# Kernel optimization log

Measured on AMD Instinct MI355X. Metric: run time of the kernel, lower is better.

The kernel has to match this reference:

```python
import jax, jax.numpy as jnp
import numpy as np
from jax import lax


def _kaiming_uniform(key, shape):
    fan_in = shape[1]
    bound = np.sqrt(6.0 / fan_in)
    return jax.random.uniform(key, shape, jnp.float32, -bound, bound)


def rbf_conv(x, w, k, pad):
    # x: [B,C,H,W]; w: [O, C*k*k]. Equivalent to F.unfold + torch.cdist (p=2).
    patches = lax.conv_general_dilated_patches(
        x, (k, k), (1, 1), [(pad, pad), (pad, pad)])  # [B, C*k*k, Ho, Wo]
    B, D, Ho, Wo = patches.shape
    p = patches.reshape(B, D, Ho * Wo)                 # [B, D, L]
    pn = jnp.sum(p * p, axis=1)                        # [B, L]
    wn = jnp.sum(w * w, axis=1)                        # [O]
    cross = jnp.einsum('bdl,od->bol', p, w)            # [B, O, L]
    d2 = pn[:, None, :] + wn[None, :, None] - 2.0 * cross
    d = jnp.sqrt(jnp.maximum(d2, 0.0))
    return d.reshape(B, w.shape[0], Ho, Wo)


def sfm(x, alpha):
    # non-overlapping (fh,fw) blocks, elementwise alpha weight, mean-pool
    B, C, H, W = x.shape
    fh, fw = alpha.shape
    xb = x.reshape(B, C, H // fh, fh, W // fw, fw).transpose(0, 1, 2, 4, 3, 5)
    return jnp.mean(xb * alpha, axis=(-2, -1))         # [B,C,H//fh,W//fw]


def gauss_act(d, std):
    return jnp.exp(d * d / (-2.0 * std * std))


def crelu(x, bias):
    return x * (x >= bias).astype(x.dtype)


def basic_block(x, w, std, bias, alpha, k, pad):
    d = rbf_conv(x, w, k, pad)
    return sfm(crelu(gauss_act(d, std), bias), alpha)


def setup_inputs() -> dict:
    key = jax.random.key(0)
    ks = jax.random.split(key, 8)
    x = jax.random.normal(ks[0], (16, 3, 128, 128), jnp.float32)
    w1 = _kaiming_uniform(ks[1], (96, 3 * 5 * 5))
    w2 = _kaiming_uniform(ks[2], (192, 96 * 5 * 5))
    w3 = _kaiming_uniform(ks[3], (384, 192 * 3 * 3))
    alpha = jnp.linspace(0.9, 0.99, 4, dtype=jnp.float32).reshape(2, 2)
    fc_w = jax.random.normal(ks[4], (100, 384 * 32 * 32), jnp.float32) * 0.01
    fc_b = jnp.zeros((100,), jnp.float32)
    return {
        'x': x,
        'w1': w1, 'std1': jnp.array([2.0], jnp.float32), 'bias1': jnp.array([0.3], jnp.float32), 'alpha1': alpha,
        'w2': w2, 'std2': jnp.array([2.0], jnp.float32), 'bias2': jnp.array([0.3], jnp.float32), 'alpha2': alpha,
        'w3': w3, 'std3': jnp.array([2.0], jnp.float32), 'bias3': jnp.array([0.3], jnp.float32),
        'fc_w': fc_w, 'fc_b': fc_b,
    }


def reference(x, w1, std1, bias1, alpha1, w2, std2, bias2, alpha2,
              w3, std3, bias3, fc_w, fc_b):
    h = basic_block(x, w1, std1, bias1, alpha1, 5, 2)      # [16,96,64,64]
    h = basic_block(h, w2, std2, bias2, alpha2, 5, 2)      # [16,192,32,32]
    d = rbf_conv(h, w3, 3, 1)                              # [16,384,32,32]
    h = crelu(gauss_act(d, std3), bias3)
    out = h.reshape(x.shape[0], -1) @ fc_w.T + fc_b        # [16,100]
    return out
```

## Files before the change

### kernel.cpp

```cpp
#include <hip/hip_runtime.h>

#define TPB 256

typedef short bf16x8 __attribute__((ext_vector_type(8)));
typedef float f32x4 __attribute__((ext_vector_type(4)));

__device__ inline unsigned short f2bf(float f) {
    unsigned int u = __float_as_uint(f);
    unsigned int r = (u + 0x7fffu + ((u >> 16) & 1u)) >> 16;
    return (unsigned short)r;
}
__device__ inline float bf2f(unsigned short h) {
    return __uint_as_float(((unsigned int)h) << 16);
}

__device__ __forceinline__ void gl16(void* lds, const void* g) {
    __builtin_amdgcn_global_load_lds(
        (const __attribute__((address_space(1))) unsigned int*)g,
        (__attribute__((address_space(3))) unsigned int*)lds, 16, 0, 0);
}

__global__ void prep_all(const float* __restrict__ x,
                         const float* __restrict__ w1, const float* __restrict__ w2,
                         const float* __restrict__ w3,
                         unsigned short* __restrict__ xbf,
                         unsigned short* __restrict__ w1r, unsigned short* __restrict__ w2r,
                         unsigned short* __restrict__ w3r, unsigned short* __restrict__ zerob,
                         float* __restrict__ wn1, float* __restrict__ wn2,
                         float* __restrict__ wn3) {
    int bid = blockIdx.x;
    int tid = threadIdx.x;
    if (bid < 1024) {
        int idx = bid * TPB + tid;
        int b = idx >> 14, px = idx & 16383;
        const float* xb = x + (size_t)b * 3 * 16384 + px;
        float v0 = xb[0], v1 = xb[16384], v2 = xb[32768];
        ushort4 v;
        v.x = f2bf(v0); v.y = f2bf(v1); v.z = f2bf(v2);
        v.w = f2bf(v0 * v0 + v1 * v1 + v2 * v2);
        *(ushort4*)&xbf[(size_t)idx * 4] = v;
    } else if (bid < 4388) {
        int idx = (bid - 1024) * TPB + tid;
        if (idx < 13056) {
            int o = idx / 136, d = idx - o * 136;
            int tp = d >> 2, c = d & 3;
            float v = 0.f;
            if (tp < 30) {
                int ki = tp / 6, kj = tp - 6 * ki;
                if (kj < 5) v = (c < 3) ? w1[o * 75 + c * 25 + ki * 5 + kj] : -0.5f;
            }
            w1r[idx] = f2bf(v);
        } else if (idx < 492288) {
            int i = idx - 13056;
            int c = i & 31; int r = i >> 5;
            int o = r % 192; r /= 192;
            int tap = r % 26; int cg = r / 26;
            float v = 0.f;
            if (tap < 25) v = w2[((size_t)o * 96 + cg * 32 + c) * 25 + tap];
            w2r[i] = f2bf(v);
        } else if (idx < 860928) {
            int i = idx - 492288;
            int c = i & 31; int r = i >> 5;
            int o = r % 192; r /= 192;
            int tap = r % 10; int cg = r / 10;
            float v = 0.f;
            if (tap < 9) v = w3[((size_t)o * 192 + cg * 32 + c) * 9 + tap];
            w3r[i] = f2bf(v);
        } else if (idx < 860992) {
            zerob[idx - 860928] = 0;
        }
    } else {
        int o = (bid - 4388) * 4 + (tid >> 6);
        int lane = tid & 63;
        const float* row; float* dst; int D;
        if (o < 96)       { row = w1 + (size_t)o * 75;           D = 75;   dst = wn1 + o; }
        else if (o < 288) { int r = o - 96;  row = w2 + (size_t)r * 2400; D = 2400; dst = wn2 + r; }
        else              { int r = o - 288; row = w3 + (size_t)r * 1728; D = 1728; dst = wn3 + r; }
        float acc = 0.f;
        for (int i = lane; i < D; i += 64) { float v = row[i]; acc += v * v; }
        #pragma unroll
        for (int off = 32; off >= 1; off >>= 1) acc += __shfl_down(acc, off);
        if (lane == 0) *dst = acc;
    }
}

__launch_bounds__(256, 2)
__global__ void conv1_mfma(const unsigned short* __restrict__ xbf,
                           const unsigned short* __restrict__ w1r,
                           const float* __restrict__ wn,
                           const float* __restrict__ stdp, const float* __restrict__ biasp,
                           const float* __restrict__ alphap,
                           unsigned short* __restrict__ out,
                           float* __restrict__ sqout)
{
    __shared__ unsigned short in_s[22 * 20 * 4];
    __shared__ unsigned short w_s[96 * 136];

    int bid = blockIdx.x;
    int tx = bid & 7; bid >>= 3;
    int ty = bid & 7; bid >>= 3;
    int b = bid;
    int x0 = tx * 16, y0 = ty * 16;
    int tid = threadIdx.x;
    int lane = tid & 63, wv = tid >> 6;
    int col = lane & 15, kg = lane >> 4;

    for (int idx = tid; idx < 21 * 20; idx += 256) {
        int py = idx / 20, px = idx - py * 20;
        int gy = y0 - 2 + py, gx = x0 - 2 + px;
        ushort4 v = make_ushort4(0, 0, 0, 0);
        if (gy >= 0 && gy < 128 && gx >= 0 && gx < 128)
            v = *(const ushort4*)&xbf[(((size_t)b * 128 + gy) * 128 + gx) * 4];
        *(ushort4*)&in_s[idx * 4] = v;
    }
    for (int idx = tid; idx < 1632; idx += 256)
        *(bf16x8*)&w_s[idx * 8] = *(const bf16x8*)&w1r[idx * 8];
    __syncthreads();

    f32x4 acc[6][4];
    #pragma unroll
    for (int mt = 0; mt < 6; ++mt)
        #pragma unroll
        for (int n = 0; n < 4; ++n) acc[mt][n] = (f32x4){0.f, 0.f, 0.f, 0.f};

    #pragma unroll
    for (int ks = 0; ks < 4; ++ks) {
        int tap0 = ks * 8 + kg * 2;
        int ki = tap0 / 6, kj = tap0 - 6 * ki;
        bf16x8 bfrag[4];
        #pragma unroll
        for (int n = 0; n < 4; ++n) {
            int row = wv * 4 + n + ki;
            int ix = col + kj;
            const unsigned short* p = &in_s[(row * 20 + ix) * 4];
            union { bf16x8 v; uint2 u[2]; } tmp;
            tmp.u[0] = *(const uint2*)p;
            tmp.u[1] = *(const uint2*)(p + 4);
            bfrag[n] = tmp.v;
        }
        bf16x8 afrag[6];
        #pragma unroll
        for (int mt = 0; mt < 6; ++mt)
            afrag[mt] = *(const bf16x8*)&w_s[(mt * 16 + col) * 136 + ks * 32 + kg * 8];
        #pragma unroll
        for (int mt = 0; mt < 6; ++mt)
            #pragma unroll
            for (int n = 0; n < 4; ++n)
                acc[mt][n] = __builtin_amdgcn_mfma_f32_16x16x32_bf16(
                    afrag[mt], bfrag[n], acc[mt][n], 0, 0, 0);
    }

    float stdv = stdp[0], biasv = biasp[0];
    float inv2s2 = 1.f / (2.f * stdv * stdv);
    float a00 = alphap[0], a01 = alphap[1], a10 = alphap[2], a11 = alphap[3];
    int dx = col & 1;
    float ax0 = dx ? a01 : a00;
    float ax1 = dx ? a11 : a10;

    float sqa[2] = {0.f, 0.f};
    #pragma unroll
    for (int mt = 0; mt < 6; ++mt) {
        #pragma unroll
        for (int p2 = 0; p2 < 2; ++p2) {
            unsigned short res[4];
            #pragma unroll
            for (int r = 0; r < 4; ++r) {
                int o = mt * 16 + kg * 4 + r;
                float wno = wn[o];
                float d20 = fmaxf(wno - 2.f * acc[mt][2 * p2][r], 0.f);
                float d21 = fmaxf(wno - 2.f * acc[mt][2 * p2 + 1][r], 0.f);
                float g0 = __expf(-d20 * inv2s2);
                float g1 = __expf(-d21 * inv2s2);
                g0 = (g0 >= biasv) ? g0 : 0.f;
                g1 = (g1 >= biasv) ? g1 : 0.f;
                float s = ax0 * g0 + ax1 * g1;
                s += __shfl_xor(s, 1);
                res[r] = f2bf(0.25f * s);
                float vv = bf2f(res[r]);
                sqa[p2] += vv * vv;
            }
            if (dx == 0) {
                int yo = ty * 8 + wv * 2 + p2, xo = tx * 8 + (col >> 1);
                *(ushort4*)&out[(((size_t)b * 64 + yo) * 64 + xo) * 96 + mt * 16 + kg * 4] =
                    make_ushort4(res[0], res[1], res[2], res[3]);
            }
        }
    }
    #pragma unroll
    for (int p2 = 0; p2 < 2; ++p2) {
        float s = sqa[p2];
        s += __shfl_xor(s, 16);
        s += __shfl_xor(s, 32);
        if (dx == 0 && kg == 0) {
            int yo = ty * 8 + wv * 2 + p2, xo = tx * 8 + (col >> 1);
            sqout[((size_t)b * 64 + yo) * 64 + xo] = s;
        }
    }
}

__launch_bounds__(256, 2)
__global__ void conv2_mfma(const unsigned short* __restrict__ hin,
                           const unsigned short* __restrict__ wt2,
                           const float* __restrict__ sq1,
                           const float* __restrict__ wn,
                           const float* __restrict__ stdp, const float* __restrict__ biasp,
                           const float* __restrict__ alphap,
                           const unsigned short* __restrict__ zerob,
                           unsigned short* __restrict__ hout)
{
    __shared__ unsigned short in_s[240 * 32];
    __shared__ unsigned short w_s[2][2 * 192 * 32];
    __shared__ float sq_s[240];
    __shared__ int s_nz[4];

    int bid = blockIdx.x;
    int xt = bid & 3; bid >>= 2;
    int yt = bid & 7; bid >>= 3;
    int b = bid;
    int x0 = xt * 16, y0 = yt * 8;
    int tid = threadIdx.x;
    int lane = tid & 63, wid = tid >> 6;
    int wave_m = wid >> 1, wave_n = wid & 1;
    int col = lane & 15, kg = lane >> 4;
    int coly = col >> 3, colx = col & 7;

    if (tid < 240) {
        int r = tid / 20, c = tid - r * 20;
        int gy = y0 - 2 + r, gx = x0 - 2 + c;
        float v = 0.f;
        if (gy >= 0 && gy < 64 && gx >= 0 && gx < 64)
            v = sq1[((size_t)b * 64 + gy) * 64 + gx];
        sq_s[tid] = v;
    }

    f32x4 acc[6][4];
    #pragma unroll
    for (int mt = 0; mt < 6; ++mt)
        #pragma unroll
        for (int nt = 0; nt < 4; ++nt) acc[mt][nt] = (f32x4){0.f, 0.f, 0.f, 0.f};

    for (int cg = 0; cg < 3; ++cg) {
        #pragma unroll
        for (int i = 0; i < 4; ++i) {
            int chunk = tid + i * 256;
            if (chunk < 960) {
                int px = chunk >> 2, c16 = chunk & 3;
                int iy = px / 20, ix = px - iy * 20;
                int gy = y0 - 2 + iy, gx = x0 - 2 + ix;
                const void* src = (gy >= 0 && gy < 64 && gx >= 0 && gx < 64)
                    ? (const void*)&hin[(((size_t)b * 64 + gy) * 64 + gx) * 96 + cg * 32 + c16 * 8]
                    : (const void*)zerob;
                gl16(&in_s[chunk * 8], src);
            }
        }
        __syncthreads();

        unsigned int nzb = 0;
        #pragma unroll
        for (int i = 0; i < 4; ++i) {
            int chunk = tid + i * 256;
            if (chunk < 960) {
                uint4 v = *(const uint4*)&in_s[chunk * 8];
                nzb |= v.x | v.y | v.z | v.w;
            }
        }
        bool any = __any(nzb != 0);
        if (lane == 0) s_nz[wid] = any ? 1 : 0;
        __syncthreads();
        if (s_nz[0] | s_nz[1] | s_nz[2] | s_nz[3]) {
            #pragma unroll
            for (int i = 0; i < 6; ++i) {
                int chunk = tid + i * 256;
                int tp = chunk / 768, rem = chunk - tp * 768;
                gl16(&w_s[0][tp * 6144 + rem * 8],
                     &wt2[(((size_t)cg * 26 + tp) * 192) * 32 + rem * 8]);
            }
            __syncthreads();
            for (int pr = 0; pr < 13; ++pr) {
                int cur = pr & 1;
                if (pr < 12) {
                    #pragma unroll
                    for (int i = 0; i < 6; ++i) {
                        int chunk = tid + i * 256;
                        int tp = chunk / 768, rem = chunk - tp * 768;
                        gl16(&w_s[cur ^ 1][tp * 6144 + rem * 8],
                             &wt2[(((size_t)cg * 26 + (pr + 1) * 2 + tp) * 192) * 32 + rem * 8]);
                    }
                }
                #pragma unroll
                for (int t2 = 0; t2 < 2; ++t2) {
                    int tap = pr * 2 + t2;
                    int ki = tap / 5, kj = tap - 5 * ki;
                    if (tap >= 25) { ki = 0; kj = 0; }
                    bf16x8 bfrag[4], afrag[6];
                    #pragma unroll
                    for (int nt = 0; nt < 4; ++nt) {
                        int yy = 2 * nt + coly + ki;
                        int xx = wave_n * 8 + colx + kj;
                        bfrag[nt] = *(const bf16x8*)&in_s[(yy * 20 + xx) * 32 + kg * 8];
                    }
                    #pragma unroll
                    for (int mt = 0; mt < 6; ++mt)
                        afrag[mt] = *(const bf16x8*)
                            &w_s[cur][t2 * 6144 + (wave_m * 96 + mt * 16 + col) * 32 + kg * 8];
                    #pragma unroll
                    for (int mt = 0; mt < 6; ++mt)
                        #pragma unroll
                        for (int nt = 0; nt < 4; ++nt)
                            acc[mt][nt] = __builtin_amdgcn_mfma_f32_16x16x32_bf16(
                                afrag[mt], bfrag[nt], acc[mt][nt], 0, 0, 0);
                }
                __syncthreads();
            }
        }
    }

    float stdv = stdp[0], biasv = biasp[0];
    float inv2s2 = 1.f / (2.f * stdv * stdv);
    float a_own = alphap[coly * 2 + (col & 1)];
    #pragma unroll
    for (int nt = 0; nt < 4; ++nt) {
        int ly = 2 * nt + coly + 2;
        int lx = wave_n * 8 + colx + 2;
        float pnv = 0.f;
        #pragma unroll
        for (int dy = -2; dy <= 2; ++dy)
            #pragma unroll
            for (int dx2 = -2; dx2 <= 2; ++dx2)
                pnv += sq_s[(ly + dy) * 20 + (lx + dx2)];
        int x = x0 + wave_n * 8 + colx;
        int yo = (y0 >> 1) + nt;
        int xo = x >> 1;
        #pragma unroll
        for (int mt = 0; mt < 6; ++mt) {
            int ob = wave_m * 96 + mt * 16 + (kg << 2);
            unsigned short res[4];
            #pragma unroll
            for (int r = 0; r < 4; ++r) {
                float d2 = fmaxf(pnv + wn[ob + r] - 2.f * acc[mt][nt][r], 0.f);
                float g = __expf(-d2 * inv2s2);
                g = (g >= biasv) ? g : 0.f;
                g *= a_own;
                g += __shfl_xor(g, 1);
                g += __shfl_xor(g, 8);
                res[r] = f2bf(0.25f * g);
            }
            if (((col & 1) == 0) && ((col & 8) == 0)) {
                *(ushort4*)&hout[(((size_t)b * 32 + yo) * 32 + xo) * 192 + ob] =
                    make_ushort4(res[0], res[1], res[2], res[3]);
            }
        }
    }
}

__launch_bounds__(256, 2)
__global__ void conv3_mfma(const unsigned short* __restrict__ hin,
                           const unsigned short* __restrict__ wt3,
                           const float* __restrict__ wn,
                           const float* __restrict__ stdp, const float* __restrict__ biasp,
                           const unsigned short* __restrict__ zerob,
                           unsigned short* __restrict__ hout)
{
    __shared__ unsigned short in_s[180 * 32];
    __shared__ unsigned short w_s[2][2 * 96 * 32];
    __shared__ float pnacc[180];

    int bid = blockIdx.x;
    int sp = bid & 7; bid >>= 3;
    int ot = bid & 3; int b = bid >> 2;
    int x0 = (sp & 1) * 16, y0 = (sp >> 1) * 8, o0 = ot * 96;
    int tid = threadIdx.x;
    int lane = tid & 63, wid = tid >> 6;
    int om = wid >> 1, wn2 = wid & 1;
    int col = lane & 15, kg = lane >> 4;
    int coly = col >> 3, colx = col & 7;

    if (tid < 180) pnacc[tid] = 0.f;

    f32x4 acc[3][4];
    #pragma unroll
    for (int mt = 0; mt < 3; ++mt)
        #pragma unroll
        for (int nt = 0; nt < 4; ++nt) acc[mt][nt] = (f32x4){0.f, 0.f, 0.f, 0.f};

    for (int cg = 0; cg < 6; ++cg) {
        #pragma unroll
        for (int i = 0; i < 3; ++i) {
            int chunk = tid + i * 256;
            if (chunk < 720) {
                int px = chunk >> 2, c16 = chunk & 3;
                int iy = px / 18, ix = px - iy * 18;
                int gy = y0 - 1 + iy, gx = x0 - 1 + ix;
                const void* src = (gy >= 0 && gy < 32 && gx >= 0 && gx < 32)
                    ? (const void*)&hin[(((size_t)b * 32 + gy) * 32 + gx) * 192 + cg * 32 + c16 * 8]
                    : (const void*)zerob;
                gl16(&in_s[chunk * 8], src);
            }
        }
        #pragma unroll
        for (int i = 0; i < 3; ++i) {
            int chunk = tid + i * 256;
            int tp = chunk / 384, rem = chunk - tp * 384;
            gl16(&w_s[0][tp * 3072 + rem * 8],
                 &wt3[(((size_t)cg * 10 + tp) * 192 + o0) * 32 + rem * 8]);
        }
        __syncthreads();

        if (tid < 180) {
            const unsigned short* p = &in_s[tid * 32];
            float a = 0.f;
            #pragma unroll
            for (int c = 0; c < 32; c += 8) {
                bf16x8 v = *(const bf16x8*)&p[c];
                #pragma unroll
                for (int j = 0; j < 8; ++j) { float f = bf2f((unsigned short)v[j]); a += f * f; }
            }
            pnacc[tid] += a;
        }

        for (int pr = 0; pr < 5; ++pr) {
            int cur = pr & 1;
            if (pr < 4) {
                #pragma unroll
                for (int i = 0; i < 3; ++i) {
                    int chunk = tid + i * 256;
                    int tp = chunk / 384, rem = chunk - tp * 384;
                    gl16(&w_s[cur ^ 1][tp * 3072 + rem * 8],
                         &wt3[(((size_t)cg * 10 + (pr + 1) * 2 + tp) * 192 + o0) * 32 + rem * 8]);
                }
            }
            #pragma unroll
            for (int t2 = 0; t2 < 2; ++t2) {
                int tap = pr * 2 + t2;
                int ki = tap / 3, kj = tap - 3 * ki;
                if (tap >= 9) { ki = 0; kj = 0; }
                bf16x8 bfrag[4], afrag[3];
                #pragma unroll
                for (int nt = 0; nt < 4; ++nt) {
                    int yy = 2 * nt + coly + ki;
                    int xx = wn2 * 8 + colx + kj;
                    bfrag[nt] = *(const bf16x8*)&in_s[(yy * 18 + xx) * 32 + kg * 8];
                }
                #pragma unroll
                for (int mt = 0; mt < 3; ++mt)
                    afrag[mt] = *(const bf16x8*)
                        &w_s[cur][(t2 * 96 + om * 48 + mt * 16 + col) * 32 + kg * 8];
                #pragma unroll
                for (int mt = 0; mt < 3; ++mt)
                    #pragma unroll
                    for (int nt = 0; nt < 4; ++nt)
                        acc[mt][nt] = __builtin_amdgcn_mfma_f32_16x16x32_bf16(
                            afrag[mt], bfrag[nt], acc[mt][nt], 0, 0, 0);
            }
            __syncthreads();
        }
    }

    float stdv = stdp[0], biasv = biasp[0];
    float inv2s2 = 1.f / (2.f * stdv * stdv);
    #pragma unroll
    for (int nt = 0; nt < 4; ++nt) {
        int y = y0 + 2 * nt + coly;
        int x = x0 + wn2 * 8 + colx;
        int ly = 2 * nt + coly + 1, lx = wn2 * 8 + colx + 1;
        float pnv = 0.f;
        #pragma unroll
        for (int dy = -1; dy <= 1; ++dy)
            #pragma unroll
            for (int dx = -1; dx <= 1; ++dx)
                pnv += pnacc[(ly + dy) * 18 + (lx + dx)];
        #pragma unroll
        for (int mt = 0; mt < 3; ++mt) {
            int ob = o0 + om * 48 + mt * 16 + (kg << 2);
            #pragma unroll
            for (int r = 0; r < 4; ++r) {
                float d2 = fmaxf(pnv + wn[ob + r] - 2.f * acc[mt][nt][r], 0.f);
                float g = __expf(-d2 * inv2s2);
                g = (g >= biasv) ? g : 0.f;
                hout[((size_t)b * 384 + ob + r) * 1024 + y * 32 + x] = f2bf(g);
            }
        }
    }
}

__launch_bounds__(256, 4)
__global__ void fc_mfma(const unsigned short* __restrict__ h3bf,
                        const float* __restrict__ fw,
                        float* __restrict__ fcp,
                        int* __restrict__ flags)
{
    __shared__ unsigned short h3s[16 * 520];
    __shared__ unsigned short fws[16 * 520];
    __shared__ float red[4][16][16];
    __shared__ int s_nz[4];
    const size_t KI = 393216;
    int ch = blockIdx.x;
    int i0 = ch * 512;
    int tid = threadIdx.x;
    int lane = tid & 63, wv = tid >> 6;
    int col = lane & 15, kg = lane >> 4;

    unsigned int nzbits = 0;
    #pragma unroll
    for (int it = 0; it < 4; ++it) {
        int c = tid + it * 256;
        int b = c >> 6, off = (c & 63) * 8;
        bf16x8 v = *(const bf16x8*)&h3bf[(size_t)b * KI + i0 + off];
        union { bf16x8 s; unsigned int u[4]; } cv; cv.s = v;
        nzbits |= cv.u[0] | cv.u[1] | cv.u[2] | cv.u[3];
        *(bf16x8*)&h3s[b * 520 + off] = v;
    }
    bool any = __any(nzbits != 0);
    if (lane == 0) s_nz[wv] = any ? 1 : 0;
    __syncthreads();
    int anyall = s_nz[0] | s_nz[1] | s_nz[2] | s_nz[3];
    if (!anyall) {
        if (tid == 0) flags[ch] = 0;
        return;
    }
    if (tid == 0) flags[ch] = 1;

    float4 pre[8];
    #pragma unroll
    for (int it = 0; it < 8; ++it) {
        int c = tid + it * 256;
        int row = c >> 7, off4 = (c & 127) * 4;
        pre[it] = (row < 100) ? *(const float4*)&fw[(size_t)row * KI + i0 + off4]
                              : make_float4(0.f, 0.f, 0.f, 0.f);
    }

    for (int jt = 0; jt < 7; ++jt) {
        int j0 = jt * 16;
        #pragma unroll
        for (int it = 0; it < 8; ++it) {
            int c = tid + it * 256;
            int row = c >> 7, off4 = (c & 127) * 4;
            *(ushort4*)&fws[row * 520 + off4] =
                make_ushort4(f2bf(pre[it].x), f2bf(pre[it].y), f2bf(pre[it].z), f2bf(pre[it].w));
        }
        if (jt < 6) {
            #pragma unroll
            for (int it = 0; it < 8; ++it) {
                int c = tid + it * 256;
                int row = c >> 7, off4 = (c & 127) * 4;
                int j = j0 + 16 + row;
                pre[it] = (j < 100) ? *(const float4*)&fw[(size_t)j * KI + i0 + off4]
                                    : make_float4(0.f, 0.f, 0.f, 0.f);
            }
        }
        __syncthreads();
        f32x4 acc = (f32x4){0.f, 0.f, 0.f, 0.f};
        #pragma unroll
        for (int s = 0; s < 4; ++s) {
            int k = wv * 128 + s * 32 + kg * 8;
            bf16x8 af = *(const bf16x8*)&fws[col * 520 + k];
            bf16x8 bg = *(const bf16x8*)&h3s[col * 520 + k];
            acc = __builtin_amdgcn_mfma_f32_16x16x32_bf16(af, bg, acc, 0, 0, 0);
        }
        #pragma unroll
        for (int r = 0; r < 4; ++r) red[wv][kg * 4 + r][col] = acc[r];
        __syncthreads();
        int j = tid >> 4, bb = tid & 15;
        float s = red[0][j][bb] + red[1][j][bb] + red[2][j][bb] + red[3][j][bb];
        fcp[((size_t)ch * 112 + j0 + j) * 16 + bb] = s;
    }
}

__global__ void fc_final(const float* __restrict__ fcp, const int* __restrict__ flags,
                         const float* __restrict__ fb, float* __restrict__ outp) {
    int j = blockIdx.x;
    int lane = threadIdx.x;
    float acc[16];
    #pragma unroll
    for (int b = 0; b < 16; ++b) acc[b] = 0.f;
    for (int ch = lane; ch < 768; ch += 64) {
        if (flags[ch]) {
            const float* p = &fcp[((size_t)ch * 112 + j) * 16];
            #pragma unroll
            for (int b = 0; b < 16; ++b) acc[b] += p[b];
        }
    }
    #pragma unroll
    for (int off = 32; off >= 1; off >>= 1)
        #pragma unroll
        for (int b = 0; b < 16; ++b) acc[b] += __shfl_down(acc[b], off);
    if (lane == 0) {
        float bj = fb[j];
        #pragma unroll
        for (int b = 0; b < 16; ++b) outp[b * 100 + j] = bj + acc[b];
    }
}

extern "C" void kernel_launch(void* const* d_in, const int* in_sizes, int n_in,
                              void* d_out, int out_size, void* d_ws, size_t ws_size,
                              hipStream_t stream) {
    const float* x      = (const float*)d_in[0];
    const float* w1     = (const float*)d_in[1];
    const float* std1   = (const float*)d_in[2];
    const float* bias1  = (const float*)d_in[3];
    const float* alpha1 = (const float*)d_in[4];
    const float* w2     = (const float*)d_in[5];
    const float* std2   = (const float*)d_in[6];
    const float* bias2  = (const float*)d_in[7];
    const float* alpha2 = (const float*)d_in[8];
    const float* w3     = (const float*)d_in[9];
    const float* std3   = (const float*)d_in[10];
    const float* bias3  = (const float*)d_in[11];
    const float* fc_w   = (const float*)d_in[12];
    const float* fc_b   = (const float*)d_in[13];
    float* out = (float*)d_out;
    float* ws  = (float*)d_ws;

    float* sbuf  = ws;
    float* fcp   = sbuf + 65536;
    float* wn1   = fcp + 1376256;
    float* wn2   = wn1 + 96;
    float* wn3   = wn2 + 192;
    int*   flags = (int*)(wn3 + 384);
    float* rest  = wn3 + 384 + 768 + 32;
    unsigned short* h1bf = (unsigned short*)rest;
    unsigned short* h2bf = h1bf + 6291456;
    unsigned short* h3bf = h2bf + 3145728;
    unsigned short* xbf  = h3bf + 6291456;
    unsigned short* w1r  = xbf + 1048576;
    unsigned short* w2r  = w1r + 13056;
    unsigned short* w3r  = w2r + 479232;
    unsigned short* zerob = w3r + 368640;

    dim3 B(TPB);

    prep_all<<<dim3(4556), B, 0, stream>>>(x, w1, w2, w3, xbf, w1r, w2r, w3r, zerob,
                                           wn1, wn2, wn3);

    conv1_mfma<<<dim3(1024), B, 0, stream>>>(xbf, w1r, wn1, std1, bias1, alpha1,
                                             h1bf, sbuf);

    conv2_mfma<<<dim3(512), B, 0, stream>>>(
        h1bf, w2r, sbuf, wn2, std2, bias2, alpha2, zerob, h2bf);

    conv3_mfma<<<dim3(512), B, 0, stream>>>(
        h2bf, w3r, wn3, std3, bias3, zerob, h3bf);

    fc_mfma<<<dim3(768), B, 0, stream>>>(h3bf, fc_w, fcp, flags);
    fc_final<<<dim3(100), dim3(64), 0, stream>>>(fcp, flags, fc_b, out);
}
```

Before: 100.9 us.

## Fuse all stages into one cooperative persistent kernel with grid syncs

Replaces the six separate kernel launches with a single cooperative megakernel of 512 blocks that runs prep, conv1, conv2, conv3, fc and the final reduction, using grid.sync between stages. Shared memory becomes one byte buffer carved per stage. The goal is to remove launch gaps and tail effects between kernels. In exchange, every stage runs with a fixed grid and occupancy, and the per-stage LDS is sized to the largest stage. If the cooperative launch fails, it falls back to separate kernels.

```diff
diff --git a/kernel.cpp b/kernel.cpp
--- a/kernel.cpp
+++ b/kernel.cpp
@@ -1,4 +1,7 @@
 #include <hip/hip_runtime.h>
+#include <hip/hip_cooperative_groups.h>
+
+namespace cg = cooperative_groups;
 
 #define TPB 256
 
@@ -20,28 +23,26 @@
         (__attribute__((address_space(3))) unsigned int*)lds, 16, 0, 0);
 }
 
-__global__ void prep_all(const float* __restrict__ x,
-                         const float* __restrict__ w1, const float* __restrict__ w2,
-                         const float* __restrict__ w3,
-                         unsigned short* __restrict__ xbf,
-                         unsigned short* __restrict__ w1r, unsigned short* __restrict__ w2r,
-                         unsigned short* __restrict__ w3r, unsigned short* __restrict__ zerob,
-                         float* __restrict__ wn1, float* __restrict__ wn2,
-                         float* __restrict__ wn3) {
-    int bid = blockIdx.x;
-    int tid = threadIdx.x;
-    if (bid < 1024) {
-        int idx = bid * TPB + tid;
-        int b = idx >> 14, px = idx & 16383;
-        const float* xb = x + (size_t)b * 3 * 16384 + px;
-        float v0 = xb[0], v1 = xb[16384], v2 = xb[32768];
-        ushort4 v;
-        v.x = f2bf(v0); v.y = f2bf(v1); v.z = f2bf(v2);
-        v.w = f2bf(v0 * v0 + v1 * v1 + v2 * v2);
-        *(ushort4*)&xbf[(size_t)idx * 4] = v;
-    } else if (bid < 4388) {
-        int idx = (bid - 1024) * TPB + tid;
-        if (idx < 13056) {
+
+__device__ __forceinline__ void dev_prep(int gi, int stride,
+    const float* __restrict__ x, const float* __restrict__ w1,
+    const float* __restrict__ w2, const float* __restrict__ w3,
+    unsigned short* __restrict__ xbf, unsigned short* __restrict__ w1r,
+    unsigned short* __restrict__ w2r, unsigned short* __restrict__ w3r,
+    unsigned short* __restrict__ zerob)
+{
+    const int NX = 262144, E1 = NX + 13056, E2 = E1 + 479232, E3 = E2 + 368640, TOT = E3 + 64;
+    for (int i = gi; i < TOT; i += stride) {
+        if (i < NX) {
+            int b = i >> 14, px = i & 16383;
+            const float* xb = x + (size_t)b * 49152 + px;
+            float v0 = xb[0], v1 = xb[16384], v2 = xb[32768];
+            ushort4 v;
+            v.x = f2bf(v0); v.y = f2bf(v1); v.z = f2bf(v2);
+            v.w = f2bf(v0 * v0 + v1 * v1 + v2 * v2);
+            *(ushort4*)&xbf[(size_t)i * 4] = v;
+        } else if (i < E1) {
+            int idx = i - NX;
             int o = idx / 136, d = idx - o * 136;
             int tp = d >> 2, c = d & 3;
             float v = 0.f;
@@ -50,58 +51,59 @@
                 if (kj < 5) v = (c < 3) ? w1[o * 75 + c * 25 + ki * 5 + kj] : -0.5f;
             }
             w1r[idx] = f2bf(v);
-        } else if (idx < 492288) {
-            int i = idx - 13056;
-            int c = i & 31; int r = i >> 5;
+        } else if (i < E2) {
+            int idx = i - E1;
+            int c = idx & 31; int r = idx >> 5;
             int o = r % 192; r /= 192;
-            int tap = r % 26; int cg = r / 26;
+            int tap = r % 26; int cgx = r / 26;
             float v = 0.f;
-            if (tap < 25) v = w2[((size_t)o * 96 + cg * 32 + c) * 25 + tap];
-            w2r[i] = f2bf(v);
-        } else if (idx < 860928) {
-            int i = idx - 492288;
-            int c = i & 31; int r = i >> 5;
+            if (tap < 25) v = w2[((size_t)o * 96 + cgx * 32 + c) * 25 + tap];
+            w2r[idx] = f2bf(v);
+        } else if (i < E3) {
+            int idx = i - E2;
+            int c = idx & 31; int r = idx >> 5;
             int o = r % 192; r /= 192;
-            int tap = r % 10; int cg = r / 10;
+            int tap = r % 10; int cgx = r / 10;
             float v = 0.f;
-            if (tap < 9) v = w3[((size_t)o * 192 + cg * 32 + c) * 9 + tap];
-            w3r[i] = f2bf(v);
-        } else if (idx < 860992) {
-            zerob[idx - 860928] = 0;
-        }
-    } else {
-        int o = (bid - 4388) * 4 + (tid >> 6);
-        int lane = tid & 63;
-        const float* row; float* dst; int D;
-        if (o < 96)       { row = w1 + (size_t)o * 75;           D = 75;   dst = wn1 + o; }
-        else if (o < 288) { int r = o - 96;  row = w2 + (size_t)r * 2400; D = 2400; dst = wn2 + r; }
-        else              { int r = o - 288; row = w3 + (size_t)r * 1728; D = 1728; dst = wn3 + r; }
-        float acc = 0.f;
-        for (int i = lane; i < D; i += 64) { float v = row[i]; acc += v * v; }
-        #pragma unroll
-        for (int off = 32; off >= 1; off >>= 1) acc += __shfl_down(acc, off);
-        if (lane == 0) *dst = acc;
-    }
-}
-
-__launch_bounds__(256, 2)
-__global__ void conv1_mfma(const unsigned short* __restrict__ xbf,
-                           const unsigned short* __restrict__ w1r,
-                           const float* __restrict__ wn,
-                           const float* __restrict__ stdp, const float* __restrict__ biasp,
-                           const float* __restrict__ alphap,
-                           unsigned short* __restrict__ out,
-                           float* __restrict__ sqout)
+            if (tap < 9) v = w3[((size_t)o * 192 + cgx * 32 + c) * 9 + tap];
+            w3r[idx] = f2bf(v);
+        } else {
+            zerob[i - E3] = 0;
+        }
+    }
+}
+
+__device__ __forceinline__ void dev_wn(int o, int lane,
+    const float* __restrict__ w1, const float* __restrict__ w2,
+    const float* __restrict__ w3,
+    float* __restrict__ wn1, float* __restrict__ wn2, float* __restrict__ wn3)
 {
-    __shared__ unsigned short in_s[22 * 20 * 4];
-    __shared__ unsigned short w_s[96 * 136];
-
-    int bid = blockIdx.x;
-    int tx = bid & 7; bid >>= 3;
-    int ty = bid & 7; bid >>= 3;
-    int b = bid;
+    const float* row; float* dst; int D;
+    if (o < 96)       { row = w1 + (size_t)o * 75;           D = 75;   dst = wn1 + o; }
+    else if (o < 288) { int r = o - 96;  row = w2 + (size_t)r * 2400; D = 2400; dst = wn2 + r; }
+    else              { int r = o - 288; row = w3 + (size_t)r * 1728; D = 1728; dst = wn3 + r; }
+    float acc = 0.f;
+    for (int i = lane; i < D; i += 64) { float v = row[i]; acc += v * v; }
+    #pragma unroll
+    for (int off = 32; off >= 1; off >>= 1) acc += __shfl_down(acc, off);
+    if (lane == 0) *dst = acc;
+}
+
+__device__ __forceinline__ void dev_conv1(int t, int tid, unsigned char* smem,
+    const unsigned short* __restrict__ xbf, const unsigned short* __restrict__ w1r,
+    const float* __restrict__ wn,
+    const float* __restrict__ stdp, const float* __restrict__ biasp,
+    const float* __restrict__ alphap,
+    unsigned short* __restrict__ out, float* __restrict__ sqout)
+{
+    unsigned short* in_s = (unsigned short*)smem;
+    unsigned short* w_s  = (unsigned short*)(smem + 3520);
+    __syncthreads();
+
+    int tx = t & 7; t >>= 3;
+    int ty = t & 7; t >>= 3;
+    int b = t;
     int x0 = tx * 16, y0 = ty * 16;
-    int tid = threadIdx.x;
     int lane = tid & 63, wv = tid >> 6;
     int col = lane & 15, kg = lane >> 4;
 
@@ -198,27 +200,22 @@
     }
 }
 
-__launch_bounds__(256, 2)
-__global__ void conv2_mfma(const unsigned short* __restrict__ hin,
-                           const unsigned short* __restrict__ wt2,
-                           const float* __restrict__ sq1,
-                           const float* __restrict__ wn,
-                           const float* __restrict__ stdp, const float* __restrict__ biasp,
-                           const float* __restrict__ alphap,
-                           const unsigned short* __restrict__ zerob,
-                           unsigned short* __restrict__ hout)
+__device__ __forceinline__ void dev_conv2(int t, int tid, unsigned char* smem,
+    const unsigned short* __restrict__ hin, const unsigned short* __restrict__ wt2,
+    const float* __restrict__ sq1, const float* __restrict__ wn,
+    const float* __restrict__ stdp, const float* __restrict__ biasp,
+    const float* __restrict__ alphap, const unsigned short* __restrict__ zerob,
+    unsigned short* __restrict__ hout)
 {
-    __shared__ unsigned short in_s[240 * 32];
-    __shared__ unsigned short w_s[2][2 * 192 * 32];
-    __shared__ float sq_s[240];
-    __shared__ int s_nz[4];
-
-    int bid = blockIdx.x;
-    int xt = bid & 3; bid >>= 2;
-    int yt = bid & 7; bid >>= 3;
-    int b = bid;
+    unsigned short* in_s = (unsigned short*)smem;
+    unsigned short* w_s  = (unsigned short*)(smem + 15360);
+    float* sq_s          = (float*)(smem + 64512);
+    int* s_nz            = (int*)(smem + 65472);
+
+    int xt = t & 3; t >>= 2;
+    int yt = t & 7; t >>= 3;
+    int b = t;
     int x0 = xt * 16, y0 = yt * 8;
-    int tid = threadIdx.x;
     int lane = tid & 63, wid = tid >> 6;
     int wave_m = wid >> 1, wave_n = wid & 1;
     int col = lane & 15, kg = lane >> 4;
@@ -239,7 +236,7 @@
         #pragma unroll
         for (int nt = 0; nt < 4; ++nt) acc[mt][nt] = (f32x4){0.f, 0.f, 0.f, 0.f};
 
-    for (int cg = 0; cg < 3; ++cg) {
+    for (int cgx = 0; cgx < 3; ++cgx) {
         #pragma unroll
         for (int i = 0; i < 4; ++i) {
             int chunk = tid + i * 256;
@@ -248,7 +245,7 @@
                 int iy = px / 20, ix = px - iy * 20;
                 int gy = y0 - 2 + iy, gx = x0 - 2 + ix;
                 const void* src = (gy >= 0 && gy < 64 && gx >= 0 && gx < 64)
-                    ? (const void*)&hin[(((size_t)b * 64 + gy) * 64 + gx) * 96 + cg * 32 + c16 * 8]
+                    ? (const void*)&hin[(((size_t)b * 64 + gy) * 64 + gx) * 96 + cgx * 32 + c16 * 8]
                     : (const void*)zerob;
                 gl16(&in_s[chunk * 8], src);
             }
@@ -272,8 +269,8 @@
             for (int i = 0; i < 6; ++i) {
                 int chunk = tid + i * 256;
                 int tp = chunk / 768, rem = chunk - tp * 768;
-                gl16(&w_s[0][tp * 6144 + rem * 8],
-                     &wt2[(((size_t)cg * 26 + tp) * 192) * 32 + rem * 8]);
+                gl16(&w_s[tp * 6144 + rem * 8],
+                     &wt2[(((size_t)cgx * 26 + tp) * 192) * 32 + rem * 8]);
             }
             __syncthreads();
             for (int pr = 0; pr < 13; ++pr) {
@@ -283,8 +280,8 @@
                     for (int i = 0; i < 6; ++i) {
                         int chunk = tid + i * 256;
                         int tp = chunk / 768, rem = chunk - tp * 768;
-                        gl16(&w_s[cur ^ 1][tp * 6144 + rem * 8],
-                             &wt2[(((size_t)cg * 26 + (pr + 1) * 2 + tp) * 192) * 32 + rem * 8]);
+                        gl16(&w_s[(cur ^ 1) * 12288 + tp * 6144 + rem * 8],
+                             &wt2[(((size_t)cgx * 26 + (pr + 1) * 2 + tp) * 192) * 32 + rem * 8]);
                     }
                 }
                 #pragma unroll
@@ -302,7 +299,7 @@
                     #pragma unroll
                     for (int mt = 0; mt < 6; ++mt)
                         afrag[mt] = *(const bf16x8*)
-                            &w_s[cur][t2 * 6144 + (wave_m * 96 + mt * 16 + col) * 32 + kg * 8];
+                            &w_s[cur * 12288 + t2 * 6144 + (wave_m * 96 + mt * 16 + col) * 32 + kg * 8];
                     #pragma unroll
                     for (int mt = 0; mt < 6; ++mt)
                         #pragma unroll
@@ -353,23 +350,19 @@
     }
 }
 
-__launch_bounds__(256, 2)
-__global__ void conv3_mfma(const unsigned short* __restrict__ hin,
-                           const unsigned short* __restrict__ wt3,
-                           const float* __restrict__ wn,
-                           const float* __restrict__ stdp, const float* __restrict__ biasp,
-                           const unsigned short* __restrict__ zerob,
-                           unsigned short* __restrict__ hout)
+__device__ __forceinline__ void dev_conv3(int t, int tid, unsigned char* smem,
+    const unsigned short* __restrict__ hin, const unsigned short* __restrict__ wt3,
+    const float* __restrict__ wn,
+    const float* __restrict__ stdp, const float* __restrict__ biasp,
+    const unsigned short* __restrict__ zerob, unsigned short* __restrict__ hout)
 {
-    __shared__ unsigned short in_s[180 * 32];
-    __shared__ unsigned short w_s[2][2 * 96 * 32];
-    __shared__ float pnacc[180];
-
-    int bid = blockIdx.x;
-    int sp = bid & 7; bid >>= 3;
-    int ot = bid & 3; int b = bid >> 2;
+    unsigned short* in_s = (unsigned short*)smem;
+    unsigned short* w_s  = (unsigned short*)(smem + 11520);
+    float* pnacc         = (float*)(smem + 36096);
+
+    int sp = t & 7; t >>= 3;
+    int ot = t & 3; int b = t >> 2;
     int x0 = (sp & 1) * 16, y0 = (sp >> 1) * 8, o0 = ot * 96;
-    int tid = threadIdx.x;
     int lane = tid & 63, wid = tid >> 6;
     int om = wid >> 1, wn2 = wid & 1;
     int col = lane & 15, kg = lane >> 4;
@@ -383,7 +376,7 @@
         #pragma unroll
         for (int nt = 0; nt < 4; ++nt) acc[mt][nt] = (f32x4){0.f, 0.f, 0.f, 0.f};
 
-    for (int cg = 0; cg < 6; ++cg) {
+    for (int cgx = 0; cgx < 6; ++cgx) {
         #pragma unroll
         for (int i = 0; i < 3; ++i) {
             int chunk = tid + i * 256;
@@ -392,7 +385,7 @@
                 int iy = px / 18, ix = px - iy * 18;
                 int gy = y0 - 1 + iy, gx = x0 - 1 + ix;
                 const void* src = (gy >= 0 && gy < 32 && gx >= 0 && gx < 32)
-                    ? (const void*)&hin[(((size_t)b * 32 + gy) * 32 + gx) * 192 + cg * 32 + c16 * 8]
+                    ? (const void*)&hin[(((size_t)b * 32 + gy) * 32 + gx) * 192 + cgx * 32 + c16 * 8]
                     : (const void*)zerob;
                 gl16(&in_s[chunk * 8], src);
             }
@@ -401,8 +394,8 @@
         for (int i = 0; i < 3; ++i) {
             int chunk = tid + i * 256;
             int tp = chunk / 384, rem = chunk - tp * 384;
-            gl16(&w_s[0][tp * 3072 + rem * 8],
-                 &wt3[(((size_t)cg * 10 + tp) * 192 + o0) * 32 + rem * 8]);
+            gl16(&w_s[tp * 3072 + rem * 8],
+                 &wt3[(((size_t)cgx * 10 + tp) * 192 + o0) * 32 + rem * 8]);
         }
         __syncthreads();
 
@@ -425,8 +418,8 @@
                 for (int i = 0; i < 3; ++i) {
                     int chunk = tid + i * 256;
                     int tp = chunk / 384, rem = chunk - tp * 384;
-                    gl16(&w_s[cur ^ 1][tp * 3072 + rem * 8],
-                         &wt3[(((size_t)cg * 10 + (pr + 1) * 2 + tp) * 192 + o0) * 32 + rem * 8]);
+                    gl16(&w_s[(cur ^ 1) * 6144 + tp * 3072 + rem * 8],
+                         &wt3[(((size_t)cgx * 10 + (pr + 1) * 2 + tp) * 192 + o0) * 32 + rem * 8]);
                 }
             }
             #pragma unroll
@@ -444,7 +437,7 @@
                 #pragma unroll
                 for (int mt = 0; mt < 3; ++mt)
                     afrag[mt] = *(const bf16x8*)
-                        &w_s[cur][(t2 * 96 + om * 48 + mt * 16 + col) * 32 + kg * 8];
+                        &w_s[cur * 6144 + t2 * 3072 + (om * 48 + mt * 16 + col) * 32 + kg * 8];
                 #pragma unroll
                 for (int mt = 0; mt < 3; ++mt)
                     #pragma unroll
@@ -483,20 +476,18 @@
     }
 }
 
-__launch_bounds__(256, 4)
-__global__ void fc_mfma(const unsigned short* __restrict__ h3bf,
-                        const float* __restrict__ fw,
-                        float* __restrict__ fcp,
-                        int* __restrict__ flags)
+__device__ __forceinline__ void dev_fc(int ch, int tid, unsigned char* smem,
+    const unsigned short* __restrict__ h3bf, const float* __restrict__ fw,
+    float* __restrict__ fcp, int* __restrict__ flags)
 {
-    __shared__ unsigned short h3s[16 * 520];
-    __shared__ unsigned short fws[16 * 520];
-    __shared__ float red[4][16][16];
-    __shared__ int s_nz[4];
+    unsigned short* h3s = (unsigned short*)smem;
+    unsigned short* fws = (unsigned short*)(smem + 16640);
+    float* red          = (float*)(smem + 33280);
+    int* s_nz           = (int*)(smem + 37376);
+    __syncthreads();
+
     const size_t KI = 393216;
-    int ch = blockIdx.x;
     int i0 = ch * 512;
-    int tid = threadIdx.x;
     int lane = tid & 63, wv = tid >> 6;
     int col = lane & 15, kg = lane >> 4;
 
@@ -558,18 +549,19 @@
             acc = __builtin_amdgcn_mfma_f32_16x16x32_bf16(af, bg, acc, 0, 0, 0);
         }
         #pragma unroll
-        for (int r = 0; r < 4; ++r) red[wv][kg * 4 + r][col] = acc[r];
+        for (int r = 0; r < 4; ++r) red[wv * 256 + (kg * 4 + r) * 16 + col] = acc[r];
         __syncthreads();
         int j = tid >> 4, bb = tid & 15;
-        float s = red[0][j][bb] + red[1][j][bb] + red[2][j][bb] + red[3][j][bb];
+        float s = red[0 * 256 + j * 16 + bb] + red[1 * 256 + j * 16 + bb] +
+                  red[2 * 256 + j * 16 + bb] + red[3 * 256 + j * 16 + bb];
         fcp[((size_t)ch * 112 + j0 + j) * 16 + bb] = s;
     }
 }
 
-__global__ void fc_final(const float* __restrict__ fcp, const int* __restrict__ flags,
-                         const float* __restrict__ fb, float* __restrict__ outp) {
-    int j = blockIdx.x;
-    int lane = threadIdx.x;
+__device__ __forceinline__ void dev_final(int j, int lane,
+    const float* __restrict__ fcp, const int* __restrict__ flags,
+    const float* __restrict__ fb, float* __restrict__ outp)
+{
     float acc[16];
     #pragma unroll
     for (int b = 0; b < 16; ++b) acc[b] = 0.f;
@@ -589,6 +581,93 @@
         #pragma unroll
         for (int b = 0; b < 16; ++b) outp[b * 100 + j] = bj + acc[b];
     }
+}
+
+__launch_bounds__(256, 2)
+__global__ void mega(const float* x, const float* w1, const float* w2, const float* w3,
+                     const float* std1, const float* bias1, const float* alpha1,
+                     const float* std2, const float* bias2, const float* alpha2,
+                     const float* std3, const float* bias3,
+                     const float* fc_w, const float* fc_b, float* out,
+                     float* sbuf, float* fcp, float* wn1, float* wn2, float* wn3,
+                     int* flags,
+                     unsigned short* h1bf, unsigned short* h2bf, unsigned short* h3bf,
+                     unsigned short* xbf, unsigned short* w1r, unsigned short* w2r,
+                     unsigned short* w3r, unsigned short* zerob)
+{
+    __shared__ __align__(16) unsigned char smem[65488];
+    cg::grid_group grid = cg::this_grid();
+    int bid = blockIdx.x;
+    int tid = threadIdx.x;
+
+    dev_prep(bid * 256 + tid, 512 * 256, x, w1, w2, w3, xbf, w1r, w2r, w3r, zerob);
+    if (bid < 168) dev_wn(bid * 4 + (tid >> 6), tid & 63, w1, w2, w3, wn1, wn2, wn3);
+    grid.sync();
+
+    for (int t = bid; t < 1024; t += 512)
+        dev_conv1(t, tid, smem, xbf, w1r, wn1, std1, bias1, alpha1, h1bf, sbuf);
+    grid.sync();
+
+    dev_conv2(bid, tid, smem, h1bf, w2r, sbuf, wn2, std2, bias2, alpha2, zerob, h2bf);
+    grid.sync();
+
+    dev_conv3(bid, tid, smem, h2bf, w3r, wn3, std3, bias3, zerob, h3bf);
+    grid.sync();
+
+    for (int ch = bid; ch < 768; ch += 512)
+        dev_fc(ch, tid, smem, h3bf, fc_w, fcp, flags);
+    grid.sync();
+
+    if (bid < 100 && tid < 64)
+        dev_final(bid, tid, fcp, flags, fc_b, out);
+}
+
+__launch_bounds__(256)
+__global__ void k_prep(const float* x, const float* w1, const float* w2, const float* w3,
+                       unsigned short* xbf, unsigned short* w1r, unsigned short* w2r,
+                       unsigned short* w3r, unsigned short* zerob,
+                       float* wn1, float* wn2, float* wn3) {
+    dev_prep(blockIdx.x * 256 + threadIdx.x, 2048 * 256, x, w1, w2, w3,
+             xbf, w1r, w2r, w3r, zerob);
+    if (blockIdx.x < 168)
+        dev_wn(blockIdx.x * 4 + (threadIdx.x >> 6), threadIdx.x & 63,
+               w1, w2, w3, wn1, wn2, wn3);
+}
+
+__launch_bounds__(256, 2)
+__global__ void k_conv1(const unsigned short* xbf, const unsigned short* w1r,
+                        const float* wn, const float* stdp, const float* biasp,
+                        const float* alphap, unsigned short* out, float* sqout) {
+    __shared__ __align__(16) unsigned char smem[29696];
+    dev_conv1(blockIdx.x, threadIdx.x, smem, xbf, w1r, wn, stdp, biasp, alphap, out, sqout);
+}
+
+__launch_bounds__(256, 2)
+__global__ void k_conv2(const unsigned short* hin, const unsigned short* wt2,
+                        const float* sq1, const float* wn, const float* stdp,
+                        const float* biasp, const float* alphap,
+                        const unsigned short* zerob, unsigned short* hout) {
+    __shared__ __align__(16) unsigned char smem[65488];
+    dev_conv2(blockIdx.x, threadIdx.x, smem, hin, wt2, sq1, wn, stdp, biasp, alphap,
+              zerob, hout);
+}
+
+__launch_bounds__(256, 2)
+__global__ void k_conv3(const unsigned short* hin, const unsigned short* wt3,
+                        const float* wn, const float* stdp, const float* biasp,
+                        const unsigned short* zerob, unsigned short* hout) {
+    __shared__ __align__(16) unsigned char smem[36864];
+    dev_conv3(blockIdx.x, threadIdx.x, smem, hin, wt3, wn, stdp, biasp, zerob, hout);
+}
+
+__launch_bounds__(256, 2)
+__global__ void k_fc(const unsigned short* h3bf, const float* fw, float* fcp, int* flags) {
+    __shared__ __align__(16) unsigned char smem[37392];
+    dev_fc(blockIdx.x, threadIdx.x, smem, h3bf, fw, fcp, flags);
+}
+
+__global__ void k_final(const float* fcp, const int* flags, const float* fb, float* outp) {
+    dev_final(blockIdx.x, threadIdx.x, fcp, flags, fb, outp);
 }
 
 extern "C" void kernel_launch(void* const* d_in, const int* in_sizes, int n_in,
@@ -627,20 +706,29 @@
     unsigned short* w3r  = w2r + 479232;
     unsigned short* zerob = w3r + 368640;
 
-    dim3 B(TPB);
-
-    prep_all<<<dim3(4556), B, 0, stream>>>(x, w1, w2, w3, xbf, w1r, w2r, w3r, zerob,
-                                           wn1, wn2, wn3);
-
-    conv1_mfma<<<dim3(1024), B, 0, stream>>>(xbf, w1r, wn1, std1, bias1, alpha1,
-                                             h1bf, sbuf);
-
-    conv2_mfma<<<dim3(512), B, 0, stream>>>(
-        h1bf, w2r, sbuf, wn2, std2, bias2, alpha2, zerob, h2bf);
-
-    conv3_mfma<<<dim3(512), B, 0, stream>>>(
-        h2bf, w3r, wn3, std3, bias3, zerob, h3bf);
-
-    fc_mfma<<<dim3(768), B, 0, stream>>>(h3bf, fc_w, fcp, flags);
-    fc_final<<<dim3(100), dim3(64), 0, stream>>>(fcp, flags, fc_b, out);
-}
+    void* args[] = {
+        (void*)&x, (void*)&w1, (void*)&w2, (void*)&w3,
+        (void*)&std1, (void*)&bias1, (void*)&alpha1,
+        (void*)&std2, (void*)&bias2, (void*)&alpha2,
+        (void*)&std3, (void*)&bias3,
+        (void*)&fc_w, (void*)&fc_b, (void*)&out,
+        (void*)&sbuf, (void*)&fcp, (void*)&wn1, (void*)&wn2, (void*)&wn3,
+        (void*)&flags,
+        (void*)&h1bf, (void*)&h2bf, (void*)&h3bf,
+        (void*)&xbf, (void*)&w1r, (void*)&w2r, (void*)&w3r, (void*)&zerob
+    };
+    hipError_t err = hipLaunchCooperativeKernel((const void*)mega, dim3(512), dim3(256),
+                                                args, 0, stream);
+    if (err != hipSuccess) {
+        dim3 B(TPB);
+        k_prep<<<dim3(2048), B, 0, stream>>>(x, w1, w2, w3, xbf, w1r, w2r, w3r, zerob,
+                                             wn1, wn2, wn3);
+        k_conv1<<<dim3(1024), B, 0, stream>>>(xbf, w1r, wn1, std1, bias1, alpha1,
+                                              h1bf, sbuf);
+        k_conv2<<<dim3(512), B, 0, stream>>>(h1bf, w2r, sbuf, wn2, std2, bias2, alpha2,
+                                             zerob, h2bf);
+        k_conv3<<<dim3(512), B, 0, stream>>>(h2bf, w3r, wn3, std3, bias3, zerob, h3bf);
+        k_fc<<<dim3(768), B, 0, stream>>>(h3bf, fc_w, fcp, flags);
+        k_final<<<dim3(100), dim3(64), 0, stream>>>(fcp, flags, fc_b, out);
+    }
+}
```

New measurement: 394.2 us. +290.6%, slower.
